# Performance work log

Measured on AMD Instinct MI355X. Metric: run time of the kernel, lower is better.

## Reference

```python
import jax, jax.numpy as jnp
import numpy as np
from jax import lax

B, C, T, V = 16, 3, 256, 25
MID = 48
DILS = (1, 2, 3, 4)
NB = len(DILS)
OUT = MID * NB
FH = [10, 100, 10, 1]
CH = [100]
EPS = 1e-5


def setup_inputs() -> dict:
    key = jax.random.key(0)
    ks = iter(jax.random.split(key, 64))
    nrm = lambda shape, s=0.05: jax.random.normal(next(ks), shape, jnp.float32) * s
    inp = {}
    inp['x'] = jax.random.normal(next(ks), (B, C, T, V), jnp.float32)
    # stacked per-timestep branch conv weights: (branch, v, mid, in=V, k=3)
    inp['Wb'] = nrm((NB, V, MID, V, 3))
    inp['bb'] = nrm((NB, V, MID))
    dims = [C] + FH
    for i in range(4):
        inp[f'fw{i}'] = nrm((dims[i + 1], dims[i]))
        inp[f'fb{i}'] = nrm((dims[i + 1],))
        inp[f'fg{i}'] = jnp.ones((dims[i + 1],), jnp.float32)
        inp[f'fbe{i}'] = jnp.zeros((dims[i + 1],), jnp.float32)
    cdims = [V] + CH + [OUT]
    for i in range(2):
        inp[f'cw{i}'] = nrm((cdims[i + 1], cdims[i]))
        inp[f'cb{i}'] = nrm((cdims[i + 1],))
        inp[f'cg{i}'] = jnp.ones((cdims[i + 1],), jnp.float32)
        inp[f'cbe{i}'] = jnp.zeros((cdims[i + 1],), jnp.float32)
    inp['Ww'] = nrm((V, OUT))  # branches_follow 1x1 conv weights (per v)
    inp['bw'] = nrm((V,))
    return inp


def _bn2d(y, g, b):
    m = y.mean((0, 2, 3), keepdims=True)
    v = ((y - m) ** 2).mean((0, 2, 3), keepdims=True)
    return g[None, :, None, None] * (y - m) / jnp.sqrt(v + EPS) + b[None, :, None, None]


def _bn1d(y, g, b):
    m = y.mean((0, 2), keepdims=True)
    v = ((y - m) ** 2).mean((0, 2), keepdims=True)
    return g[None, :, None] * (y - m) / jnp.sqrt(v + EPS) + b[None, :, None]


def reference(x, Wb, bb, fw0, fb0, fg0, fbe0, fw1, fb1, fg1, fbe1,
              fw2, fb2, fg2, fbe2, fw3, fb3, fg3, fbe3,
              cw0, cb0, cg0, cbe0, cw1, cb1, cg1, cbe1, Ww, bw):
    N = B * C
    x_temp = x.reshape(N, T, V).transpose(0, 2, 1)  # (N, V, T)
    # --- branches: 25 convs per branch fused as one big conv (out = V*MID) ---
    outs = []
    for i, d in enumerate(DILS):
        pad = 2 * d  # k + (k-1)(d-1) - 1 with k=3
        kern = Wb[i].reshape(V * MID, V, 3)
        y = lax.conv_general_dilated(x_temp, kern, window_strides=(1,),
                                     padding=[(pad, 0)], rhs_dilation=(d,),
                                     dimension_numbers=('NCH', 'OIH', 'NCH'))
        y = y + bb[i].reshape(V * MID)[None, :, None]  # (N, V*MID, T)
        # torch.cat over the 25 convs along time -> (N, MID, V*T)
        y = y.reshape(N, V, MID, T).transpose(0, 2, 1, 3).reshape(N, MID, V * T)
        outs.append(y)
    predic = jnp.stack(outs)  # (NB, N, MID, V*T)
    predic = predic.transpose(1, 0, 2, 3).reshape(N, NB * MID, V * T)
    predic = predic.reshape(N, -1, T, V).reshape(B, C, OUT, T, V)
    # --- feature branches (1x1 Conv2d + BN + ReLU chain) ---
    h = x
    for w, bi, g, be in ((fw0, fb0, fg0, fbe0), (fw1, fb1, fg1, fbe1),
                         (fw2, fb2, fg2, fbe2), (fw3, fb3, fg3, fbe3)):
        h = jnp.einsum('bctv,oc->botv', h, w) + bi[None, :, None, None]
        h = jax.nn.relu(_bn2d(h, g, be))
    h = h.reshape(-1, T, V).transpose(0, 2, 1).mean(-1, keepdims=True)  # (B, V, 1)
    # --- causal branches (1x1 Conv1d + BN + ReLU) ---
    for w, bi, g, be in ((cw0, cb0, cg0, cbe0), (cw1, cb1, cg1, cbe1)):
        h = jnp.einsum('bcl,oc->bol', h, w) + bi[None, :, None]
        h = jax.nn.relu(_bn1d(h, g, be))
    xg = h[:, :, :, None]  # (B, OUT, 1, 1)
    # --- gate, relu, per-timestep follow convs ---
    predic = predic * xg[:, None]  # (B, C, OUT, T, V)
    predic = jax.nn.relu(predic.reshape(N, OUT, T, V))
    predic_final = jnp.einsum('notv,vo->nvt', predic, Ww) + bw[None, :, None]  # (N, V, T)
    predic_loss = (predic_final[:, :, :-1] - x_temp[:, :, 1:]) ** 2  # MSE, no reduction
    # --- GC pool + regularization ---
    gc_pool = Wb.transpose(0, 2, 1, 3, 4).reshape(OUT, V, V, 3)
    gcw = gc_pool[None] * xg[:, :, :, :, None]  # (B, OUT, V, V, 3)
    lam = jnp.float32(0.01)
    reg = lam * (jnp.sum(jnp.sqrt(jnp.sum(gcw ** 2, axis=(1, 4)))) +
                 jnp.sum(jnp.sqrt(jnp.sum(gcw ** 2, axis=1))))
    gc = gcw.max(axis=1).max(axis=-1)  # (B, V, V)
    return (predic_loss, gc, reg)
```

## Files before the change

kernel.cpp:

```cpp
#include <hip/hip_runtime.h>

#define EPSV 1e-5f

constexpr int kB = 16, kC = 3, kT = 256, kV = 25;
constexpr int kMID = 48, kNB = 4, kOUT = 192, kN = 48;
constexpr int kS  = kB * kT * kV;
constexpr int kTV = kT * kV;

typedef __attribute__((ext_vector_type(8))) short bf16x8;
typedef __attribute__((ext_vector_type(4))) float f32x4;

__device__ __forceinline__ short f2bf(float f) {
  unsigned u = __float_as_uint(f);
  u += 0x7fffu + ((u >> 16) & 1u);
  return (short)(u >> 16);
}
__device__ __forceinline__ float bf2f(short s) {
  return __uint_as_float(((unsigned)(unsigned short)s) << 16);
}
__device__ __forceinline__ float wred(float v) {
  #pragma unroll
  for (int d = 32; d > 0; d >>= 1) v += __shfl_xor(v, d);
  return v;
}

__global__ __launch_bounds__(128) void xmom_kernel(const float* __restrict__ x,
                                                   float* __restrict__ xmom)
{
  __shared__ float red[9];
  const int tid = threadIdx.x;
  if (tid < 9) red[tid] = 0.f;
  __syncthreads();
  const int s = blockIdx.x * 128 + tid;
  const int b = s / kTV, r = s - b * kTV;
  const float x0 = x[(b * 3 + 0) * kTV + r];
  const float x1 = x[(b * 3 + 1) * kTV + r];
  const float x2 = x[(b * 3 + 2) * kTV + r];
  const float p[9] = {x0, x1, x2, x0*x0, x0*x1, x0*x2, x1*x1, x1*x2, x2*x2};
  #pragma unroll
  for (int k = 0; k < 9; k++) {
    float t = wred(p[k]);
    if ((tid & 63) == 0) atomicAdd(&red[k], t);
  }
  __syncthreads();
  if (tid < 9) atomicAdd(&xmom[tid], red[tid]);
}

__device__ __forceinline__ void st0_from_xmom(int o, const float* fw0, const float* fb0,
                                              const float* fg0, const float* fbe0,
                                              const float* xmom, float* sc0, float* sh0)
{
  float w0 = fw0[o * 3], w1 = fw0[o * 3 + 1], w2 = fw0[o * 3 + 2], b = fb0[o];
  float Sw = w0 * xmom[0] + w1 * xmom[1] + w2 * xmom[2];
  float Q  = w0*w0*xmom[3] + w1*w1*xmom[6] + w2*w2*xmom[8]
           + 2.f*(w0*w1*xmom[4] + w0*w2*xmom[5] + w1*w2*xmom[7]);
  float mean = (Sw + (float)kS * b) * (1.f / kS);
  float e2   = (Q + 2.f * b * Sw) * (1.f / kS) + b * b;
  float var  = e2 - mean * mean;
  float sc   = fg0[o] * rsqrtf(var + EPSV);
  sc0[o] = sc; sh0[o] = fbe0[o] - mean * sc;
}

__global__ __launch_bounds__(128) void h0mom_kernel(
    const float* __restrict__ x,
    const float* __restrict__ fw0, const float* __restrict__ fb0,
    const float* __restrict__ fg0, const float* __restrict__ fbe0,
    const float* __restrict__ xmom, float* __restrict__ h0mom)
{
  __shared__ __align__(16) float w0p[40];
  __shared__ float sc0[10], sh0[10];
  __shared__ float red[65];
  const int tid = threadIdx.x;
  for (int j = tid; j < 40; j += 128) {
    int o = j >> 2, c = j & 3;
    w0p[j] = (c < 3) ? fw0[o * 3 + c] : fb0[o];
  }
  if (tid < 10) st0_from_xmom(tid, fw0, fb0, fg0, fbe0, xmom, sc0, sh0);
  if (tid < 65) red[tid] = 0.f;
  __syncthreads();
  const int s = blockIdx.x * 128 + tid;
  const int b = s / kTV, r = s - b * kTV;
  const float x0 = x[(b * 3 + 0) * kTV + r];
  const float x1 = x[(b * 3 + 1) * kTV + r];
  const float x2 = x[(b * 3 + 2) * kTV + r];
  float h0[10];
  #pragma unroll
  for (int o = 0; o < 10; o++) {
    const float4 w = *(const float4*)&w0p[o * 4];
    float y = fmaf(x0, w.x, fmaf(x1, w.y, fmaf(x2, w.z, w.w)));
    h0[o] = fmaxf(fmaf(y, sc0[o], sh0[o]), 0.f);
  }
  int idx = 0;
  #pragma unroll
  for (int c = 0; c < 10; c++) {
    float t = wred(h0[c]);
    if ((tid & 63) == 0) atomicAdd(&red[idx], t);
    idx++;
  }
  #pragma unroll
  for (int c = 0; c < 10; c++)
    #pragma unroll
    for (int cp = c; cp < 10; cp++) {
      float t = wred(h0[c] * h0[cp]);
      if ((tid & 63) == 0) atomicAdd(&red[idx], t);
      idx++;
    }
  __syncthreads();
  if (tid < 65) atomicAdd(&h0mom[tid], red[tid]);
}

__global__ __launch_bounds__(128) void y2_kernel(
    const float* __restrict__ x,
    const float* __restrict__ fw0, const float* __restrict__ fb0,
    const float* __restrict__ fg0, const float* __restrict__ fbe0,
    const float* __restrict__ fw1, const float* __restrict__ fb1,
    const float* __restrict__ fg1, const float* __restrict__ fbe1,
    const float* __restrict__ fw2, const float* __restrict__ fb2,
    const float* __restrict__ xmom, const float* __restrict__ h0mom,
    short* __restrict__ y2out, float* __restrict__ st2out)
{
  __shared__ __align__(16) float w0p[40];
  __shared__ __align__(16) float w1p[1200];
  __shared__ __align__(16) float w2t[1200];
  __shared__ float b2s[10];
  __shared__ float sc0[10], sh0[10], sc1[100], sh1[100];
  __shared__ float red[20];
  const int tid = threadIdx.x;

  for (int j = tid; j < 40; j += 128) {
    int o = j >> 2, c = j & 3;
    w0p[j] = (c < 3) ? fw0[o * 3 + c] : fb0[o];
  }
  for (int j = tid; j < 1200; j += 128) {
    int o = j / 12, c = j - o * 12;
    w1p[j] = (c < 10) ? fw1[o * 10 + c] : (c == 10 ? fb1[o] : 0.f);
  }
  for (int j = tid; j < 1000; j += 128) {
    int jj = j / 100, c = j - jj * 100;
    w2t[c * 12 + jj] = fw2[j];
  }
  for (int c = tid; c < 100; c += 128) { w2t[c * 12 + 10] = 0.f; w2t[c * 12 + 11] = 0.f; }
  if (tid < 10) {
    b2s[tid] = fb2[tid];
    st0_from_xmom(tid, fw0, fb0, fg0, fbe0, xmom, sc0, sh0);
  }
  if (tid < 20) red[tid] = 0.f;
  __syncthreads();
  if (tid < 100) {
    float wr[10]; float S = 0.f, Q = 0.f;
    #pragma unroll
    for (int c = 0; c < 10; c++) { wr[c] = w1p[tid * 12 + c]; S = fmaf(wr[c], h0mom[c], S); }
    int idx = 10;
    #pragma unroll
    for (int c = 0; c < 10; c++) {
      Q = fmaf(wr[c] * wr[c], h0mom[idx], Q); idx++;
      #pragma unroll
      for (int cp = c + 1; cp < 10; cp++) { Q = fmaf(2.f * wr[c] * wr[cp], h0mom[idx], Q); idx++; }
    }
    float b = w1p[tid * 12 + 10];
    float mean = (S + (float)kS * b) * (1.f / kS);
    float e2   = (Q + 2.f * b * S) * (1.f / kS) + b * b;
    float var  = e2 - mean * mean;
    float sc   = fg1[tid] * rsqrtf(var + EPSV);
    sc1[tid] = sc; sh1[tid] = fbe1[tid] - mean * sc;
  }
  __syncthreads();

  const int s0 = blockIdx.x * 512 + tid;
  float h0a[4][10];
  #pragma unroll
  for (int k = 0; k < 4; k++) {
    const int s = s0 + k * 128;
    const int b = s / kTV, r = s - b * kTV;
    const float x0 = x[(b * 3 + 0) * kTV + r];
    const float x1 = x[(b * 3 + 1) * kTV + r];
    const float x2 = x[(b * 3 + 2) * kTV + r];
    #pragma unroll
    for (int o = 0; o < 10; o++) {
      const float4 w = *(const float4*)&w0p[o * 4];
      float y = fmaf(x0, w.x, fmaf(x1, w.y, fmaf(x2, w.z, w.w)));
      h0a[k][o] = fmaxf(fmaf(y, sc0[o], sh0[o]), 0.f);
    }
  }
  float acc[4][10];
  #pragma unroll
  for (int k = 0; k < 4; k++)
    #pragma unroll
    for (int o = 0; o < 10; o++) acc[k][o] = b2s[o];

  #pragma unroll 2
  for (int o = 0; o < 100; o++) {
    const float4 wa = *(const float4*)&w1p[o * 12];
    const float4 wb = *(const float4*)&w1p[o * 12 + 4];
    const float4 wc = *(const float4*)&w1p[o * 12 + 8];
    const float4 va = *(const float4*)&w2t[o * 12];
    const float4 vb = *(const float4*)&w2t[o * 12 + 4];
    const float4 vc = *(const float4*)&w2t[o * 12 + 8];
    const float sc = sc1[o], sh = sh1[o];
    #pragma unroll
    for (int k = 0; k < 4; k++) {
      float a = wc.z;
      a = fmaf(h0a[k][0], wa.x, a); a = fmaf(h0a[k][1], wa.y, a);
      a = fmaf(h0a[k][2], wa.z, a); a = fmaf(h0a[k][3], wa.w, a);
      a = fmaf(h0a[k][4], wb.x, a); a = fmaf(h0a[k][5], wb.y, a);
      a = fmaf(h0a[k][6], wb.z, a); a = fmaf(h0a[k][7], wb.w, a);
      a = fmaf(h0a[k][8], wc.x, a); a = fmaf(h0a[k][9], wc.y, a);
      const float h1 = fmaxf(fmaf(a, sc, sh), 0.f);
      acc[k][0] = fmaf(h1, va.x, acc[k][0]); acc[k][1] = fmaf(h1, va.y, acc[k][1]);
      acc[k][2] = fmaf(h1, va.z, acc[k][2]); acc[k][3] = fmaf(h1, va.w, acc[k][3]);
      acc[k][4] = fmaf(h1, vb.x, acc[k][4]); acc[k][5] = fmaf(h1, vb.y, acc[k][5]);
      acc[k][6] = fmaf(h1, vb.z, acc[k][6]); acc[k][7] = fmaf(h1, vb.w, acc[k][7]);
      acc[k][8] = fmaf(h1, vc.x, acc[k][8]); acc[k][9] = fmaf(h1, vc.y, acc[k][9]);
    }
  }

  #pragma unroll
  for (int k = 0; k < 4; k++) {
    const int s = s0 + k * 128;
    #pragma unroll
    for (int o = 0; o < 10; o++) y2out[o * kS + s] = f2bf(acc[k][o]);
  }
  #pragma unroll
  for (int o = 0; o < 10; o++) {
    float s1 = acc[0][o] + acc[1][o] + acc[2][o] + acc[3][o];
    float s2 = acc[0][o]*acc[0][o] + acc[1][o]*acc[1][o] + acc[2][o]*acc[2][o] + acc[3][o]*acc[3][o];
    s1 = wred(s1); s2 = wred(s2);
    if ((tid & 63) == 0) { atomicAdd(&red[2 * o], s1); atomicAdd(&red[2 * o + 1], s2); }
  }
  __syncthreads();
  if (tid < 20) atomicAdd(&st2out[tid], red[tid]);
}

__global__ __launch_bounds__(128) void y3_kernel(
    const short* __restrict__ y2,
    const float* __restrict__ fw3, const float* __restrict__ fb3,
    const float* __restrict__ fg2, const float* __restrict__ fbe2,
    const float* __restrict__ st2,
    float* __restrict__ y3out, float* __restrict__ st3out)
{
  __shared__ float sc2[10], sh2[10], w3s[10];
  __shared__ float b3s;
  __shared__ float red[2];
  const int tid = threadIdx.x;
  if (tid < 10) {
    float m  = st2[2 * tid] * (1.f / kS);
    float vr = st2[2 * tid + 1] * (1.f / kS) - m * m;
    float sc = fg2[tid] * rsqrtf(vr + EPSV);
    sc2[tid] = sc; sh2[tid] = fbe2[tid] - m * sc;
    w3s[tid] = fw3[tid];
  }
  if (tid == 0) b3s = fb3[0];
  if (tid < 2) red[tid] = 0.f;
  __syncthreads();
  const int s = blockIdx.x * 128 + tid;
  float y3 = b3s;
  #pragma unroll
  for (int o = 0; o < 10; o++) {
    float v = bf2f(y2[o * kS + s]);
    float h2 = fmaxf(fmaf(v, sc2[o], sh2[o]), 0.f);
    y3 = fmaf(h2, w3s[o], y3);
  }
  y3out[s] = y3;
  float s1 = wred(y3), s2 = wred(y3 * y3);
  if ((tid & 63) == 0) { atomicAdd(&red[0], s1); atomicAdd(&red[1], s2); }
  __syncthreads();
  if (tid < 2) atomicAdd(&st3out[tid], red[tid]);
}

__global__ __launch_bounds__(128) void pool5_kernel(
    const float* __restrict__ y3,
    const float* __restrict__ fg3, const float* __restrict__ fbe3,
    const float* __restrict__ st3, float* __restrict__ hp)
{
  __shared__ float scsh[2];
  __shared__ float poolp[25];
  const int tid = threadIdx.x;
  if (tid == 0) {
    float m  = st3[0] * (1.f / kS);
    float vr = st3[1] * (1.f / kS) - m * m;
    float sc = fg3[0] * rsqrtf(vr + EPSV);
    scsh[0] = sc; scsh[1] = fbe3[0] - m * sc;
  }
  if (tid < 25) poolp[tid] = 0.f;
  __syncthreads();
  const int s = blockIdx.x * 128 + tid;
  const int b = s / kTV, r = s - b * kTV;
  const int v = r % 25;
  float h3 = fmaxf(fmaf(y3[s], scsh[0], scsh[1]), 0.f);
  atomicAdd(&poolp[v], h3);
  __syncthreads();
  if (tid < 25) atomicAdd(&hp[b * 25 + tid], poolp[tid]);
}

__global__ __launch_bounds__(256) void head_kernel(
    const float* __restrict__ hp,
    const float* __restrict__ cw0, const float* __restrict__ cb0,
    const float* __restrict__ cg0, const float* __restrict__ cbe0,
    const float* __restrict__ cw1, const float* __restrict__ cb1,
    const float* __restrict__ cg1, const float* __restrict__ cbe1,
    float* __restrict__ xg, float* __restrict__ xgT)
{
  __shared__ float hpl[400];
  __shared__ float y1[100 * 16];
  __shared__ float y2l[192 * 16];
  const int tid = threadIdx.x;
  for (int j = tid; j < 400; j += 256) hpl[j] = hp[j] * (1.f / kT);
  __syncthreads();
  for (int j = tid; j < 1600; j += 256) {
    int o = j >> 4, b = j & 15;
    float acc = cb0[o];
    for (int v = 0; v < 25; v++) acc = fmaf(hpl[b * 25 + v], cw0[o * 25 + v], acc);
    y1[o * 16 + b] = acc;
  }
  __syncthreads();
  if (tid < 100) {
    float s1 = 0.f, s2 = 0.f;
    for (int b = 0; b < 16; b++) { float val = y1[tid * 16 + b]; s1 += val; s2 += val * val; }
    float m = s1 * (1.f / 16), vr = s2 * (1.f / 16) - m * m;
    float scale = cg0[tid] * rsqrtf(vr + EPSV);
    float shift = cbe0[tid] - m * scale;
    for (int b = 0; b < 16; b++)
      y1[tid * 16 + b] = fmaxf(fmaf(y1[tid * 16 + b], scale, shift), 0.f);
  }
  __syncthreads();
  for (int j = tid; j < 3072; j += 256) {
    int o = j >> 4, b = j & 15;
    float acc = cb1[o];
    for (int c = 0; c < 100; c++) acc = fmaf(y1[c * 16 + b], cw1[o * 100 + c], acc);
    y2l[o * 16 + b] = acc;
  }
  __syncthreads();
  if (tid < 192) {
    float s1 = 0.f, s2 = 0.f;
    for (int b = 0; b < 16; b++) { float val = y2l[tid * 16 + b]; s1 += val; s2 += val * val; }
    float m = s1 * (1.f / 16), vr = s2 * (1.f / 16) - m * m;
    float scale = cg1[tid] * rsqrtf(vr + EPSV);
    float shift = cbe1[tid] - m * scale;
    for (int b = 0; b < 16; b++) {
      float r = fmaxf(fmaf(y2l[tid * 16 + b], scale, shift), 0.f);
      xg[b * 192 + tid]  = r;
      xgT[tid * 16 + b]  = r;
    }
  }
}

__global__ __launch_bounds__(256) void conv_fuse_mfma(
    const float* __restrict__ x, const float* __restrict__ Wb,
    const float* __restrict__ bb, const float* __restrict__ Ww,
    const float* __restrict__ bw, const float* __restrict__ xg,
    float* __restrict__ out_loss)
{
  __shared__ short xs[264 * 40];
  __shared__ short As[48 * 104];
  __shared__ float gw[25 * 200];
  __shared__ float bbl[192], bwl[32];

  const int tid = threadIdx.x;
  const int v = blockIdx.x % 25, n = blockIdx.x / 25;
  const int bidx = n / 3;

  {
    uint2* p = (uint2*)xs;
    for (int j = tid; j < 2640; j += 256) p[j] = make_uint2(0u, 0u);
    uint2* p2 = (uint2*)As;
    for (int j = tid; j < 1248; j += 256) p2[j] = make_uint2(0u, 0u);
  }
  __syncthreads();
  for (int j = tid; j < 6400; j += 256) {
    int t = j / 25, ci = j - t * 25;
    xs[(8 + t) * 40 + ci] = f2bf(x[n * 6400 + j]);
  }
  for (int j = tid; j < 4800; j += 256) {
    int vv = j / 192, o = j - vv * 192;
    gw[vv * 200 + o] = xg[bidx * 192 + o] * Ww[j];
  }
  for (int j = tid; j < 192; j += 256) {
    int i = j / 48, m = j - i * 48;
    bbl[j] = bb[(i * 25 + v) * 48 + m];
  }
  if (tid < 25) bwl[tid] = bw[tid];

  const int lane = tid & 63, w = tid >> 6;
  const int c = lane & 15, q = lane >> 4;

  float accout[4] = {0.f, 0.f, 0.f, 0.f};
  int tarr[4], vparr[4];
  #pragma unroll
  for (int z = 0; z < 4; z++) {
    int t = (w * 4 + z) * 16 + c;
    tarr[z] = t;
    vparr[z] = (v * 256 + t) % 25;
  }

  for (int i = 0; i < 4; i++) {
    __syncthreads();
    const float* wsrc = Wb + (i * 25 + v) * 3600;
    for (int j = tid; j < 3600; j += 256) {
      int m = j / 75, r = j - m * 75;
      int ci = r / 3, k = r - ci * 3;
      As[m * 104 + k * 32 + ci] = f2bf(wsrc[j]);
    }
    __syncthreads();

    const int d = i + 1;
    bf16x8 af[3][3];
    #pragma unroll
    for (int mt = 0; mt < 3; mt++)
      #pragma unroll
      for (int s = 0; s < 3; s++)
        af[mt][s] = *(const bf16x8*)&As[(mt * 16 + c) * 104 + s * 32 + q * 8];

    #pragma unroll
    for (int z = 0; z < 4; z++) {
      const int t = tarr[z];
      bf16x8 bf[3];
      #pragma unroll
      for (int s = 0; s < 3; s++) {
        int row = 8 + t + (s - 2) * d;
        bf[s] = *(const bf16x8*)&xs[row * 40 + q * 8];
      }
      f32x4 acc[3] = {{0.f,0.f,0.f,0.f},{0.f,0.f,0.f,0.f},{0.f,0.f,0.f,0.f}};
      #pragma unroll
      for (int s = 0; s < 3; s++)
        #pragma unroll
        for (int mt = 0; mt < 3; mt++)
          acc[mt] = __builtin_amdgcn_mfma_f32_16x16x32_bf16(af[mt][s], bf[s], acc[mt], 0, 0, 0);
      const int vp = vparr[z];
      float aout = 0.f;
      #pragma unroll
      for (int mt = 0; mt < 3; mt++) {
        #pragma unroll
        for (int r = 0; r < 4; r++) {
          int o = i * 48 + mt * 16 + q * 4 + r;
          float val = acc[mt][r] + bbl[o];
          aout = fmaf(fmaxf(val, 0.f), gw[vp * 200 + o], aout);
        }
      }
      accout[z] += aout;
    }
  }

  #pragma unroll
  for (int z = 0; z < 4; z++) {
    float a = accout[z];
    a += __shfl_xor(a, 16);
    a += __shfl_xor(a, 32);
    if (q == 0) {
      int flat = v * 256 + tarr[z];
      int tp = flat / 25, vp = flat - tp * 25;
      if (tp < 255) {
        float pf = a + bwl[vp];
        float xn = x[n * 6400 + (tp + 1) * 25 + vp];
        float dd = pf - xn;
        out_loss[(n * 25 + vp) * 255 + tp] = dd * dd;
      }
    }
  }
}

__global__ __launch_bounds__(64) void gc_reg_kernel(
    const float* __restrict__ Wb, const float* __restrict__ xgT,
    float* __restrict__ gc_out, float* __restrict__ reg_out)
{
  __shared__ float sW[576];
  __shared__ float sG[192 * 17];
  const int tid = threadIdx.x;
  const int v1 = blockIdx.x / 25, v2 = blockIdx.x % 25;
  for (int j = tid; j < 3072; j += 64) {
    int o = j >> 4, bq = j & 15;
    sG[o * 17 + bq] = xgT[j];
  }
  for (int p = tid; p < 192; p += 64) {
    int i = p / 48, m = p - i * 48;
    const float* src = Wb + ((i * 25 + v1) * 48 + m) * 75 + v2 * 3;
    sW[p * 3 + 0] = src[0]; sW[p * 3 + 1] = src[1]; sW[p * 3 + 2] = src[2];
  }
  __syncthreads();
  const int b = tid & 15, c = tid >> 4;
  float s0 = 0.f, s1 = 0.f, s2 = 0.f, mx = -3.0e38f;
  #pragma unroll 4
  for (int o = c * 48; o < c * 48 + 48; o++) {
    float g = sG[o * 17 + b];
    float a0 = sW[o * 3] * g, a1 = sW[o * 3 + 1] * g, a2 = sW[o * 3 + 2] * g;
    s0 = fmaf(a0, a0, s0);
    s1 = fmaf(a1, a1, s1);
    s2 = fmaf(a2, a2, s2);
    mx = fmaxf(mx, fmaxf(fmaxf(a0, a1), a2));
  }
  s0 += __shfl_xor(s0, 16); s0 += __shfl_xor(s0, 32);
  s1 += __shfl_xor(s1, 16); s1 += __shfl_xor(s1, 32);
  s2 += __shfl_xor(s2, 16); s2 += __shfl_xor(s2, 32);
  mx = fmaxf(mx, __shfl_xor(mx, 16)); mx = fmaxf(mx, __shfl_xor(mx, 32));
  float contrib = 0.f;
  if (c == 0) {
    gc_out[(b * 25 + v1) * 25 + v2] = mx;
    contrib = sqrtf(s0 + s1 + s2) + sqrtf(s0) + sqrtf(s1) + sqrtf(s2);
  }
  #pragma unroll
  for (int d = 1; d < 16; d <<= 1) contrib += __shfl_xor(contrib, d);
  if (tid == 0) atomicAdd(reg_out, 0.01f * contrib);
}

extern "C" void kernel_launch(void* const* d_in, const int* in_sizes, int n_in,
                              void* d_out, int out_size, void* d_ws, size_t ws_size,
                              hipStream_t stream)
{
  const float* x    = (const float*)d_in[0];
  const float* Wb   = (const float*)d_in[1];
  const float* bb   = (const float*)d_in[2];
  const float* fw0  = (const float*)d_in[3];
  const float* fb0  = (const float*)d_in[4];
  const float* fg0  = (const float*)d_in[5];
  const float* fbe0 = (const float*)d_in[6];
  const float* fw1  = (const float*)d_in[7];
  const float* fb1  = (const float*)d_in[8];
  const float* fg1  = (const float*)d_in[9];
  const float* fbe1 = (const float*)d_in[10];
  const float* fw2  = (const float*)d_in[11];
  const float* fb2  = (const float*)d_in[12];
  const float* fg2  = (const float*)d_in[13];
  const float* fbe2 = (const float*)d_in[14];
  const float* fw3  = (const float*)d_in[15];
  const float* fb3  = (const float*)d_in[16];
  const float* fg3  = (const float*)d_in[17];
  const float* fbe3 = (const float*)d_in[18];
  const float* cw0  = (const float*)d_in[19];
  const float* cb0  = (const float*)d_in[20];
  const float* cg0  = (const float*)d_in[21];
  const float* cbe0 = (const float*)d_in[22];
  const float* cw1  = (const float*)d_in[23];
  const float* cb1  = (const float*)d_in[24];
  const float* cg1  = (const float*)d_in[25];
  const float* cbe1 = (const float*)d_in[26];
  const float* Ww   = (const float*)d_in[27];
  const float* bw   = (const float*)d_in[28];

  float* ws  = (float*)d_ws;
  float* out = (float*)d_out;

  float* XMOM  = ws;
  float* H0MOM = ws + 16;
  float* ST2   = ws + 296;
  float* ST3   = ws + 316;
  float* HP    = ws + 320;
  float* XG    = ws + 768;
  float* XGT   = ws + 3840;
  short* Y2    = (short*)(ws + 8192);
  float* Y3    = ws + 520192;

  hipMemsetAsync(ws, 0, 720 * sizeof(float), stream);
  hipMemsetAsync(out + 316000, 0, sizeof(float), stream);

  xmom_kernel<<<800, 128, 0, stream>>>(x, XMOM);
  h0mom_kernel<<<800, 128, 0, stream>>>(x, fw0, fb0, fg0, fbe0, XMOM, H0MOM);
  y2_kernel<<<200, 128, 0, stream>>>(x, fw0, fb0, fg0, fbe0, fw1, fb1, fg1, fbe1,
      fw2, fb2, XMOM, H0MOM, Y2, ST2);
  y3_kernel<<<800, 128, 0, stream>>>(Y2, fw3, fb3, fg2, fbe2, ST2, Y3, ST3);
  pool5_kernel<<<800, 128, 0, stream>>>(Y3, fg3, fbe3, ST3, HP);
  head_kernel<<<1, 256, 0, stream>>>(HP, cw0, cb0, cg0, cbe0, cw1, cb1, cg1, cbe1, XG, XGT);
  conv_fuse_mfma<<<1200, 256, 0, stream>>>(x, Wb, bb, Ww, bw, XG, out);
  gc_reg_kernel<<<625, 64, 0, stream>>>(Wb, XGT, out + 306000, out + 316000);
}
```

Baseline: 165.2 us.

## Fuse pre-conv stages into one cooperative kernel with grid syncs

Merges the moment, feature-MLP, BN-stat, pooling, head and GC/regularization kernels into a single cooperative kernel of 256 blocks that uses grid.sync between stages. Y2/Y3 no longer round-trip through global memory because activations stay in registers. The same kernel also pre-converts x and Wb into padded bf16 layouts and precomputes the gated follow weights, so the MFMA conv kernel only does vector copies. This removes several launches and intermediate traffic, at the cost of grid-wide barriers, lower occupancy and serial head work on one block.

```diff
diff --git a/kernel.cpp b/kernel.cpp
--- a/kernel.cpp
+++ b/kernel.cpp
@@ -1,4 +1,7 @@
 #include <hip/hip_runtime.h>
+#include <hip/hip_cooperative_groups.h>
+
+namespace cg = cooperative_groups;
 
 #define EPSV 1e-5f
 
@@ -15,36 +18,20 @@
   u += 0x7fffu + ((u >> 16) & 1u);
   return (short)(u >> 16);
 }
-__device__ __forceinline__ float bf2f(short s) {
-  return __uint_as_float(((unsigned)(unsigned short)s) << 16);
-}
 __device__ __forceinline__ float wred(float v) {
   #pragma unroll
   for (int d = 32; d > 0; d >>= 1) v += __shfl_xor(v, d);
   return v;
 }
 
-__global__ __launch_bounds__(128) void xmom_kernel(const float* __restrict__ x,
-                                                   float* __restrict__ xmom)
-{
-  __shared__ float red[9];
-  const int tid = threadIdx.x;
-  if (tid < 9) red[tid] = 0.f;
-  __syncthreads();
-  const int s = blockIdx.x * 128 + tid;
-  const int b = s / kTV, r = s - b * kTV;
-  const float x0 = x[(b * 3 + 0) * kTV + r];
-  const float x1 = x[(b * 3 + 1) * kTV + r];
-  const float x2 = x[(b * 3 + 2) * kTV + r];
-  const float p[9] = {x0, x1, x2, x0*x0, x0*x1, x0*x2, x1*x1, x1*x2, x2*x2};
-  #pragma unroll
-  for (int k = 0; k < 9; k++) {
-    float t = wred(p[k]);
-    if ((tid & 63) == 0) atomicAdd(&red[k], t);
-  }
-  __syncthreads();
-  if (tid < 9) atomicAdd(&xmom[tid], red[tid]);
-}
+struct Params {
+  const float *x, *Wb, *bb;
+  const float *fw0,*fb0,*fg0,*fbe0, *fw1,*fb1,*fg1,*fbe1;
+  const float *fw2,*fb2,*fg2,*fbe2, *fw3,*fb3,*fg3,*fbe3;
+  const float *cw0,*cb0,*cg0,*cbe0, *cw1,*cb1,*cg1,*cbe1;
+  const float *Ww,*bw;
+  float* ws; float* out;
+};
 
 __device__ __forceinline__ void st0_from_xmom(int o, const float* fw0, const float* fb0,
                                               const float* fg0, const float* fbe0,
@@ -61,144 +48,175 @@
   sc0[o] = sc; sh0[o] = fbe0[o] - mean * sc;
 }
 
-__global__ __launch_bounds__(128) void h0mom_kernel(
-    const float* __restrict__ x,
-    const float* __restrict__ fw0, const float* __restrict__ fb0,
-    const float* __restrict__ fg0, const float* __restrict__ fbe0,
-    const float* __restrict__ xmom, float* __restrict__ h0mom)
+__global__ __launch_bounds__(256) void fused_pre(Params p)
 {
+  cg::grid_group grid = cg::this_grid();
+  const int tid = threadIdx.x, bid = blockIdx.x;
+  const int gtid = bid * 256 + tid;
+
+  float* XMOM  = p.ws;
+  float* H0MOM = p.ws + 16;
+  float* ST2   = p.ws + 112;
+  float* ST3   = p.ws + 132;
+  float* HP    = p.ws + 144;
+  float* XG    = p.ws + 544;
+  float* XGT   = p.ws + 3616;
+  float* GW    = p.ws + 8192;
+  short* WBBF  = (short*)(p.ws + 88192);
+  short* XSG   = (short*)(p.ws + 337792);
+
+  __shared__ float l_red[65];
   __shared__ __align__(16) float w0p[40];
   __shared__ float sc0[10], sh0[10];
-  __shared__ float red[65];
-  const int tid = threadIdx.x;
-  for (int j = tid; j < 40; j += 128) {
+  __shared__ __align__(16) float w1p[1200];
+  __shared__ __align__(16) float w2t[1200];
+  __shared__ float sc1[100], sh1[100];
+  __shared__ float b2s[10];
+  __shared__ float sc2[10], sh2[10], w3s[12];
+  __shared__ float st3l[2];
+  __shared__ float sG[192 * 17];
+  __shared__ float hpl[400];
+  __shared__ float y1h[1600];
+  __shared__ float y2h[3072];
+
+  for (int j = gtid; j < 48 * 10560; j += 65536) {
+    int n = j / 10560, rem = j - n * 10560;
+    int row = rem / 40, ci = rem - row * 40;
+    short val = 0;
+    if (row >= 8 && ci < 25) val = f2bf(p.x[n * 6400 + (row - 8) * 25 + ci]);
+    XSG[j] = val;
+  }
+  for (int j = gtid; j < 499200; j += 65536) {
+    int g = j / 4992, rem = j - g * 4992;
+    int m = rem / 104, kk = rem - m * 104;
+    int k = kk >> 5, ci = kk & 31;
+    short val = 0;
+    if (ci < 25 && kk < 96) val = f2bf(p.Wb[g * 3600 + m * 75 + ci * 3 + k]);
+    WBBF[j] = val;
+  }
+
+  const int s0_ = gtid, s1_ = gtid + 65536;
+  const bool ns2 = (s1_ < kS);
+  float xv[2][3] = {{0.f,0.f,0.f},{0.f,0.f,0.f}};
+  {
+    int b0 = s0_ / kTV, r0 = s0_ - b0 * kTV;
+    xv[0][0] = p.x[(b0*3+0)*kTV + r0];
+    xv[0][1] = p.x[(b0*3+1)*kTV + r0];
+    xv[0][2] = p.x[(b0*3+2)*kTV + r0];
+    if (ns2) {
+      int b1 = s1_ / kTV, r1 = s1_ - b1 * kTV;
+      xv[1][0] = p.x[(b1*3+0)*kTV + r1];
+      xv[1][1] = p.x[(b1*3+1)*kTV + r1];
+      xv[1][2] = p.x[(b1*3+2)*kTV + r1];
+    }
+  }
+  for (int j = tid; j < 9; j += 256) l_red[j] = 0.f;
+  __syncthreads();
+  {
+    float pm[9];
+    pm[0] = xv[0][0]+xv[1][0]; pm[1] = xv[0][1]+xv[1][1]; pm[2] = xv[0][2]+xv[1][2];
+    pm[3] = xv[0][0]*xv[0][0]+xv[1][0]*xv[1][0];
+    pm[4] = xv[0][0]*xv[0][1]+xv[1][0]*xv[1][1];
+    pm[5] = xv[0][0]*xv[0][2]+xv[1][0]*xv[1][2];
+    pm[6] = xv[0][1]*xv[0][1]+xv[1][1]*xv[1][1];
+    pm[7] = xv[0][1]*xv[0][2]+xv[1][1]*xv[1][2];
+    pm[8] = xv[0][2]*xv[0][2]+xv[1][2]*xv[1][2];
+    #pragma unroll
+    for (int k = 0; k < 9; k++) {
+      float t = wred(pm[k]);
+      if ((tid & 63) == 0) atomicAdd(&l_red[k], t);
+    }
+  }
+  __syncthreads();
+  if (tid < 9) atomicAdd(&XMOM[tid], l_red[tid]);
+  grid.sync();
+
+  if (tid < 10) st0_from_xmom(tid, p.fw0, p.fb0, p.fg0, p.fbe0, XMOM, sc0, sh0);
+  for (int j = tid; j < 40; j += 256) {
     int o = j >> 2, c = j & 3;
-    w0p[j] = (c < 3) ? fw0[o * 3 + c] : fb0[o];
-  }
-  if (tid < 10) st0_from_xmom(tid, fw0, fb0, fg0, fbe0, xmom, sc0, sh0);
-  if (tid < 65) red[tid] = 0.f;
-  __syncthreads();
-  const int s = blockIdx.x * 128 + tid;
-  const int b = s / kTV, r = s - b * kTV;
-  const float x0 = x[(b * 3 + 0) * kTV + r];
-  const float x1 = x[(b * 3 + 1) * kTV + r];
-  const float x2 = x[(b * 3 + 2) * kTV + r];
-  float h0[10];
+    w0p[j] = (c < 3) ? p.fw0[o * 3 + c] : p.fb0[o];
+  }
+  for (int j = tid; j < 65; j += 256) l_red[j] = 0.f;
+  __syncthreads();
+  float h0a[2][10];
   #pragma unroll
   for (int o = 0; o < 10; o++) {
     const float4 w = *(const float4*)&w0p[o * 4];
-    float y = fmaf(x0, w.x, fmaf(x1, w.y, fmaf(x2, w.z, w.w)));
-    h0[o] = fmaxf(fmaf(y, sc0[o], sh0[o]), 0.f);
-  }
-  int idx = 0;
-  #pragma unroll
-  for (int c = 0; c < 10; c++) {
-    float t = wred(h0[c]);
-    if ((tid & 63) == 0) atomicAdd(&red[idx], t);
-    idx++;
-  }
-  #pragma unroll
-  for (int c = 0; c < 10; c++)
-    #pragma unroll
-    for (int cp = c; cp < 10; cp++) {
-      float t = wred(h0[c] * h0[cp]);
-      if ((tid & 63) == 0) atomicAdd(&red[idx], t);
+    float y0 = fmaf(xv[0][0], w.x, fmaf(xv[0][1], w.y, fmaf(xv[0][2], w.z, w.w)));
+    h0a[0][o] = fmaxf(fmaf(y0, sc0[o], sh0[o]), 0.f);
+    if (ns2) {
+      float y1v = fmaf(xv[1][0], w.x, fmaf(xv[1][1], w.y, fmaf(xv[1][2], w.z, w.w)));
+      h0a[1][o] = fmaxf(fmaf(y1v, sc0[o], sh0[o]), 0.f);
+    } else h0a[1][o] = 0.f;
+  }
+  {
+    int idx = 0;
+    #pragma unroll
+    for (int c = 0; c < 10; c++) {
+      float t = wred(h0a[0][c] + h0a[1][c]);
+      if ((tid & 63) == 0) atomicAdd(&l_red[idx], t);
       idx++;
     }
-  __syncthreads();
-  if (tid < 65) atomicAdd(&h0mom[tid], red[tid]);
-}
-
-__global__ __launch_bounds__(128) void y2_kernel(
-    const float* __restrict__ x,
-    const float* __restrict__ fw0, const float* __restrict__ fb0,
-    const float* __restrict__ fg0, const float* __restrict__ fbe0,
-    const float* __restrict__ fw1, const float* __restrict__ fb1,
-    const float* __restrict__ fg1, const float* __restrict__ fbe1,
-    const float* __restrict__ fw2, const float* __restrict__ fb2,
-    const float* __restrict__ xmom, const float* __restrict__ h0mom,
-    short* __restrict__ y2out, float* __restrict__ st2out)
-{
-  __shared__ __align__(16) float w0p[40];
-  __shared__ __align__(16) float w1p[1200];
-  __shared__ __align__(16) float w2t[1200];
-  __shared__ float b2s[10];
-  __shared__ float sc0[10], sh0[10], sc1[100], sh1[100];
-  __shared__ float red[20];
-  const int tid = threadIdx.x;
-
-  for (int j = tid; j < 40; j += 128) {
-    int o = j >> 2, c = j & 3;
-    w0p[j] = (c < 3) ? fw0[o * 3 + c] : fb0[o];
-  }
-  for (int j = tid; j < 1200; j += 128) {
+    #pragma unroll
+    for (int c = 0; c < 10; c++)
+      #pragma unroll
+      for (int cp = c; cp < 10; cp++) {
+        float t = wred(h0a[0][c]*h0a[0][cp] + h0a[1][c]*h0a[1][cp]);
+        if ((tid & 63) == 0) atomicAdd(&l_red[idx], t);
+        idx++;
+      }
+  }
+  __syncthreads();
+  if (tid < 65) atomicAdd(&H0MOM[tid], l_red[tid]);
+  grid.sync();
+
+  for (int j = tid; j < 1200; j += 256) {
     int o = j / 12, c = j - o * 12;
-    w1p[j] = (c < 10) ? fw1[o * 10 + c] : (c == 10 ? fb1[o] : 0.f);
-  }
-  for (int j = tid; j < 1000; j += 128) {
+    w1p[j] = (c < 10) ? p.fw1[o * 10 + c] : (c == 10 ? p.fb1[o] : 0.f);
+  }
+  for (int j = tid; j < 1000; j += 256) {
     int jj = j / 100, c = j - jj * 100;
-    w2t[c * 12 + jj] = fw2[j];
-  }
-  for (int c = tid; c < 100; c += 128) { w2t[c * 12 + 10] = 0.f; w2t[c * 12 + 11] = 0.f; }
-  if (tid < 10) {
-    b2s[tid] = fb2[tid];
-    st0_from_xmom(tid, fw0, fb0, fg0, fbe0, xmom, sc0, sh0);
-  }
-  if (tid < 20) red[tid] = 0.f;
+    w2t[c * 12 + jj] = p.fw2[j];
+  }
+  for (int c = tid; c < 100; c += 256) { w2t[c*12+10] = 0.f; w2t[c*12+11] = 0.f; }
+  if (tid < 10) b2s[tid] = p.fb2[tid];
+  for (int j = tid; j < 20; j += 256) l_red[j] = 0.f;
   __syncthreads();
   if (tid < 100) {
     float wr[10]; float S = 0.f, Q = 0.f;
     #pragma unroll
-    for (int c = 0; c < 10; c++) { wr[c] = w1p[tid * 12 + c]; S = fmaf(wr[c], h0mom[c], S); }
+    for (int c = 0; c < 10; c++) { wr[c] = w1p[tid*12+c]; S = fmaf(wr[c], H0MOM[c], S); }
     int idx = 10;
     #pragma unroll
     for (int c = 0; c < 10; c++) {
-      Q = fmaf(wr[c] * wr[c], h0mom[idx], Q); idx++;
-      #pragma unroll
-      for (int cp = c + 1; cp < 10; cp++) { Q = fmaf(2.f * wr[c] * wr[cp], h0mom[idx], Q); idx++; }
-    }
-    float b = w1p[tid * 12 + 10];
+      Q = fmaf(wr[c]*wr[c], H0MOM[idx], Q); idx++;
+      #pragma unroll
+      for (int cp = c + 1; cp < 10; cp++) { Q = fmaf(2.f*wr[c]*wr[cp], H0MOM[idx], Q); idx++; }
+    }
+    float b = w1p[tid*12+10];
     float mean = (S + (float)kS * b) * (1.f / kS);
     float e2   = (Q + 2.f * b * S) * (1.f / kS) + b * b;
     float var  = e2 - mean * mean;
-    float sc   = fg1[tid] * rsqrtf(var + EPSV);
-    sc1[tid] = sc; sh1[tid] = fbe1[tid] - mean * sc;
-  }
-  __syncthreads();
-
-  const int s0 = blockIdx.x * 512 + tid;
-  float h0a[4][10];
-  #pragma unroll
-  for (int k = 0; k < 4; k++) {
-    const int s = s0 + k * 128;
-    const int b = s / kTV, r = s - b * kTV;
-    const float x0 = x[(b * 3 + 0) * kTV + r];
-    const float x1 = x[(b * 3 + 1) * kTV + r];
-    const float x2 = x[(b * 3 + 2) * kTV + r];
-    #pragma unroll
-    for (int o = 0; o < 10; o++) {
-      const float4 w = *(const float4*)&w0p[o * 4];
-      float y = fmaf(x0, w.x, fmaf(x1, w.y, fmaf(x2, w.z, w.w)));
-      h0a[k][o] = fmaxf(fmaf(y, sc0[o], sh0[o]), 0.f);
-    }
-  }
-  float acc[4][10];
-  #pragma unroll
-  for (int k = 0; k < 4; k++)
+    float sc   = p.fg1[tid] * rsqrtf(var + EPSV);
+    sc1[tid] = sc; sh1[tid] = p.fbe1[tid] - mean * sc;
+  }
+  __syncthreads();
+  float acc[2][10];
+  #pragma unroll
+  for (int k = 0; k < 2; k++)
     #pragma unroll
     for (int o = 0; o < 10; o++) acc[k][o] = b2s[o];
-
   #pragma unroll 2
   for (int o = 0; o < 100; o++) {
-    const float4 wa = *(const float4*)&w1p[o * 12];
-    const float4 wb = *(const float4*)&w1p[o * 12 + 4];
-    const float4 wc = *(const float4*)&w1p[o * 12 + 8];
-    const float4 va = *(const float4*)&w2t[o * 12];
-    const float4 vb = *(const float4*)&w2t[o * 12 + 4];
-    const float4 vc = *(const float4*)&w2t[o * 12 + 8];
+    const float4 wa = *(const float4*)&w1p[o*12];
+    const float4 wb = *(const float4*)&w1p[o*12+4];
+    const float4 wc = *(const float4*)&w1p[o*12+8];
+    const float4 va = *(const float4*)&w2t[o*12];
+    const float4 vb = *(const float4*)&w2t[o*12+4];
+    const float4 vc = *(const float4*)&w2t[o*12+8];
     const float sc = sc1[o], sh = sh1[o];
     #pragma unroll
-    for (int k = 0; k < 4; k++) {
+    for (int k = 0; k < 2; k++) {
       float a = wc.z;
       a = fmaf(h0a[k][0], wa.x, a); a = fmaf(h0a[k][1], wa.y, a);
       a = fmaf(h0a[k][2], wa.z, a); a = fmaf(h0a[k][3], wa.w, a);
@@ -213,146 +231,156 @@
       acc[k][8] = fmaf(h1, vc.x, acc[k][8]); acc[k][9] = fmaf(h1, vc.y, acc[k][9]);
     }
   }
-
-  #pragma unroll
-  for (int k = 0; k < 4; k++) {
-    const int s = s0 + k * 128;
-    #pragma unroll
-    for (int o = 0; o < 10; o++) y2out[o * kS + s] = f2bf(acc[k][o]);
-  }
   #pragma unroll
   for (int o = 0; o < 10; o++) {
-    float s1 = acc[0][o] + acc[1][o] + acc[2][o] + acc[3][o];
-    float s2 = acc[0][o]*acc[0][o] + acc[1][o]*acc[1][o] + acc[2][o]*acc[2][o] + acc[3][o]*acc[3][o];
-    s1 = wred(s1); s2 = wred(s2);
-    if ((tid & 63) == 0) { atomicAdd(&red[2 * o], s1); atomicAdd(&red[2 * o + 1], s2); }
-  }
-  __syncthreads();
-  if (tid < 20) atomicAdd(&st2out[tid], red[tid]);
+    float a1 = acc[0][o] + (ns2 ? acc[1][o] : 0.f);
+    float a2 = acc[0][o]*acc[0][o] + (ns2 ? acc[1][o]*acc[1][o] : 0.f);
+    a1 = wred(a1); a2 = wred(a2);
+    if ((tid & 63) == 0) { atomicAdd(&l_red[2*o], a1); atomicAdd(&l_red[2*o+1], a2); }
+  }
+  __syncthreads();
+  if (tid < 20) atomicAdd(&ST2[tid], l_red[tid]);
+  grid.sync();
+
+  if (tid < 10) {
+    float m  = ST2[2*tid] * (1.f / kS);
+    float vr = ST2[2*tid+1] * (1.f / kS) - m * m;
+    float sc = p.fg2[tid] * rsqrtf(vr + EPSV);
+    sc2[tid] = sc; sh2[tid] = p.fbe2[tid] - m * sc;
+  }
+  if (tid < 12) w3s[tid] = (tid < 10) ? p.fw3[tid] : (tid == 10 ? p.fb3[0] : 0.f);
+  if (tid < 2) l_red[tid] = 0.f;
+  __syncthreads();
+  float y3v[2];
+  #pragma unroll
+  for (int k = 0; k < 2; k++) {
+    float y3 = w3s[10];
+    #pragma unroll
+    for (int o = 0; o < 10; o++) {
+      float h2 = fmaxf(fmaf(acc[k][o], sc2[o], sh2[o]), 0.f);
+      y3 = fmaf(h2, w3s[o], y3);
+    }
+    y3v[k] = y3;
+  }
+  {
+    float a1 = y3v[0] + (ns2 ? y3v[1] : 0.f);
+    float a2 = y3v[0]*y3v[0] + (ns2 ? y3v[1]*y3v[1] : 0.f);
+    a1 = wred(a1); a2 = wred(a2);
+    if ((tid & 63) == 0) { atomicAdd(&l_red[0], a1); atomicAdd(&l_red[1], a2); }
+  }
+  __syncthreads();
+  if (tid < 2) atomicAdd(&ST3[tid], l_red[tid]);
+  grid.sync();
+
+  if (tid == 0) {
+    float m  = ST3[0] * (1.f / kS);
+    float vr = ST3[1] * (1.f / kS) - m * m;
+    float sc = p.fg3[0] * rsqrtf(vr + EPSV);
+    st3l[0] = sc; st3l[1] = p.fbe3[0] - m * sc;
+  }
+  __syncthreads();
+  {
+    int b0 = s0_ / kTV, r0 = s0_ - b0 * kTV;
+    float h3 = fmaxf(fmaf(y3v[0], st3l[0], st3l[1]), 0.f);
+    atomicAdd(&HP[b0 * 25 + r0 % 25], h3);
+    if (ns2) {
+      int b1 = s1_ / kTV, r1 = s1_ - b1 * kTV;
+      float h3b = fmaxf(fmaf(y3v[1], st3l[0], st3l[1]), 0.f);
+      atomicAdd(&HP[b1 * 25 + r1 % 25], h3b);
+    }
+  }
+  grid.sync();
+
+  if (bid == 0) {
+    for (int j = tid; j < 400; j += 256) hpl[j] = HP[j] * (1.f / kT);
+    __syncthreads();
+    for (int j = tid; j < 1600; j += 256) {
+      int o = j >> 4, b = j & 15;
+      float a = p.cb0[o];
+      for (int v = 0; v < 25; v++) a = fmaf(hpl[b*25+v], p.cw0[o*25+v], a);
+      y1h[o*16+b] = a;
+    }
+    __syncthreads();
+    if (tid < 100) {
+      float a1 = 0.f, a2 = 0.f;
+      for (int b = 0; b < 16; b++) { float val = y1h[tid*16+b]; a1 += val; a2 += val*val; }
+      float m = a1 * (1.f/16), vr = a2 * (1.f/16) - m*m;
+      float scale = p.cg0[tid] * rsqrtf(vr + EPSV);
+      float shift = p.cbe0[tid] - m * scale;
+      for (int b = 0; b < 16; b++)
+        y1h[tid*16+b] = fmaxf(fmaf(y1h[tid*16+b], scale, shift), 0.f);
+    }
+    __syncthreads();
+    for (int j = tid; j < 3072; j += 256) {
+      int o = j >> 4, b = j & 15;
+      float a = p.cb1[o];
+      for (int c = 0; c < 100; c++) a = fmaf(y1h[c*16+b], p.cw1[o*100+c], a);
+      y2h[o*16+b] = a;
+    }
+    __syncthreads();
+    if (tid < 192) {
+      float a1 = 0.f, a2 = 0.f;
+      for (int b = 0; b < 16; b++) { float val = y2h[tid*16+b]; a1 += val; a2 += val*val; }
+      float m = a1 * (1.f/16), vr = a2 * (1.f/16) - m*m;
+      float scale = p.cg1[tid] * rsqrtf(vr + EPSV);
+      float shift = p.cbe1[tid] - m * scale;
+      for (int b = 0; b < 16; b++) {
+        float r = fmaxf(fmaf(y2h[tid*16+b], scale, shift), 0.f);
+        XG[b*192+tid]  = r;
+        XGT[tid*16+b]  = r;
+      }
+    }
+  }
+  grid.sync();
+
+  for (int j = gtid; j < 80000; j += 65536) {
+    int bidx = j / 5000, rem = j - bidx * 5000;
+    int vp = rem / 200, o = rem - vp * 200;
+    GW[j] = (o < 192) ? XG[bidx*192+o] * p.Ww[vp*192+o] : 0.f;
+  }
+  for (int j = tid; j < 3072; j += 256) sG[(j>>4)*17 + (j&15)] = XGT[j];
+  __syncthreads();
+  {
+    const int lane = tid & 63, wave = tid >> 6;
+    const int u = bid * 4 + wave;
+    if (u < 625) {
+      const int v1 = u / 25, v2 = u - v1 * 25;
+      const int b = lane & 15, c = lane >> 4;
+      float q0 = 0.f, q1 = 0.f, q2 = 0.f, mx = -3.0e38f;
+      const float* wbase = p.Wb + ((c*25+v1)*48)*75 + v2*3;
+      #pragma unroll 4
+      for (int m = 0; m < 48; m++) {
+        const float* w3 = wbase + m * 75;
+        float g = sG[(c*48+m)*17 + b];
+        float a0 = w3[0]*g, a1 = w3[1]*g, a2 = w3[2]*g;
+        q0 = fmaf(a0, a0, q0); q1 = fmaf(a1, a1, q1); q2 = fmaf(a2, a2, q2);
+        mx = fmaxf(mx, fmaxf(fmaxf(a0, a1), a2));
+      }
+      q0 += __shfl_xor(q0, 16); q0 += __shfl_xor(q0, 32);
+      q1 += __shfl_xor(q1, 16); q1 += __shfl_xor(q1, 32);
+      q2 += __shfl_xor(q2, 16); q2 += __shfl_xor(q2, 32);
+      mx = fmaxf(mx, __shfl_xor(mx, 16)); mx = fmaxf(mx, __shfl_xor(mx, 32));
+      float contrib = 0.f;
+      if (c == 0) {
+        p.out[306000 + (b*25+v1)*25 + v2] = mx;
+        contrib = sqrtf(q0+q1+q2) + sqrtf(q0) + sqrtf(q1) + sqrtf(q2);
+      }
+      #pragma unroll
+      for (int d = 1; d < 16; d <<= 1) contrib += __shfl_xor(contrib, d);
+      if (lane == 0) atomicAdd(&p.out[316000], 0.01f * contrib);
+    }
+  }
 }
 
-__global__ __launch_bounds__(128) void y3_kernel(
-    const short* __restrict__ y2,
-    const float* __restrict__ fw3, const float* __restrict__ fb3,
-    const float* __restrict__ fg2, const float* __restrict__ fbe2,
-    const float* __restrict__ st2,
-    float* __restrict__ y3out, float* __restrict__ st3out)
-{
-  __shared__ float sc2[10], sh2[10], w3s[10];
-  __shared__ float b3s;
-  __shared__ float red[2];
-  const int tid = threadIdx.x;
-  if (tid < 10) {
-    float m  = st2[2 * tid] * (1.f / kS);
-    float vr = st2[2 * tid + 1] * (1.f / kS) - m * m;
-    float sc = fg2[tid] * rsqrtf(vr + EPSV);
-    sc2[tid] = sc; sh2[tid] = fbe2[tid] - m * sc;
-    w3s[tid] = fw3[tid];
-  }
-  if (tid == 0) b3s = fb3[0];
-  if (tid < 2) red[tid] = 0.f;
-  __syncthreads();
-  const int s = blockIdx.x * 128 + tid;
-  float y3 = b3s;
-  #pragma unroll
-  for (int o = 0; o < 10; o++) {
-    float v = bf2f(y2[o * kS + s]);
-    float h2 = fmaxf(fmaf(v, sc2[o], sh2[o]), 0.f);
-    y3 = fmaf(h2, w3s[o], y3);
-  }
-  y3out[s] = y3;
-  float s1 = wred(y3), s2 = wred(y3 * y3);
-  if ((tid & 63) == 0) { atomicAdd(&red[0], s1); atomicAdd(&red[1], s2); }
-  __syncthreads();
-  if (tid < 2) atomicAdd(&st3out[tid], red[tid]);
-}
-
-__global__ __launch_bounds__(128) void pool5_kernel(
-    const float* __restrict__ y3,
-    const float* __restrict__ fg3, const float* __restrict__ fbe3,
-    const float* __restrict__ st3, float* __restrict__ hp)
-{
-  __shared__ float scsh[2];
-  __shared__ float poolp[25];
-  const int tid = threadIdx.x;
-  if (tid == 0) {
-    float m  = st3[0] * (1.f / kS);
-    float vr = st3[1] * (1.f / kS) - m * m;
-    float sc = fg3[0] * rsqrtf(vr + EPSV);
-    scsh[0] = sc; scsh[1] = fbe3[0] - m * sc;
-  }
-  if (tid < 25) poolp[tid] = 0.f;
-  __syncthreads();
-  const int s = blockIdx.x * 128 + tid;
-  const int b = s / kTV, r = s - b * kTV;
-  const int v = r % 25;
-  float h3 = fmaxf(fmaf(y3[s], scsh[0], scsh[1]), 0.f);
-  atomicAdd(&poolp[v], h3);
-  __syncthreads();
-  if (tid < 25) atomicAdd(&hp[b * 25 + tid], poolp[tid]);
-}
-
-__global__ __launch_bounds__(256) void head_kernel(
-    const float* __restrict__ hp,
-    const float* __restrict__ cw0, const float* __restrict__ cb0,
-    const float* __restrict__ cg0, const float* __restrict__ cbe0,
-    const float* __restrict__ cw1, const float* __restrict__ cb1,
-    const float* __restrict__ cg1, const float* __restrict__ cbe1,
-    float* __restrict__ xg, float* __restrict__ xgT)
-{
-  __shared__ float hpl[400];
-  __shared__ float y1[100 * 16];
-  __shared__ float y2l[192 * 16];
-  const int tid = threadIdx.x;
-  for (int j = tid; j < 400; j += 256) hpl[j] = hp[j] * (1.f / kT);
-  __syncthreads();
-  for (int j = tid; j < 1600; j += 256) {
-    int o = j >> 4, b = j & 15;
-    float acc = cb0[o];
-    for (int v = 0; v < 25; v++) acc = fmaf(hpl[b * 25 + v], cw0[o * 25 + v], acc);
-    y1[o * 16 + b] = acc;
-  }
-  __syncthreads();
-  if (tid < 100) {
-    float s1 = 0.f, s2 = 0.f;
-    for (int b = 0; b < 16; b++) { float val = y1[tid * 16 + b]; s1 += val; s2 += val * val; }
-    float m = s1 * (1.f / 16), vr = s2 * (1.f / 16) - m * m;
-    float scale = cg0[tid] * rsqrtf(vr + EPSV);
-    float shift = cbe0[tid] - m * scale;
-    for (int b = 0; b < 16; b++)
-      y1[tid * 16 + b] = fmaxf(fmaf(y1[tid * 16 + b], scale, shift), 0.f);
-  }
-  __syncthreads();
-  for (int j = tid; j < 3072; j += 256) {
-    int o = j >> 4, b = j & 15;
-    float acc = cb1[o];
-    for (int c = 0; c < 100; c++) acc = fmaf(y1[c * 16 + b], cw1[o * 100 + c], acc);
-    y2l[o * 16 + b] = acc;
-  }
-  __syncthreads();
-  if (tid < 192) {
-    float s1 = 0.f, s2 = 0.f;
-    for (int b = 0; b < 16; b++) { float val = y2l[tid * 16 + b]; s1 += val; s2 += val * val; }
-    float m = s1 * (1.f / 16), vr = s2 * (1.f / 16) - m * m;
-    float scale = cg1[tid] * rsqrtf(vr + EPSV);
-    float shift = cbe1[tid] - m * scale;
-    for (int b = 0; b < 16; b++) {
-      float r = fmaxf(fmaf(y2l[tid * 16 + b], scale, shift), 0.f);
-      xg[b * 192 + tid]  = r;
-      xgT[tid * 16 + b]  = r;
-    }
-  }
-}
-
 __global__ __launch_bounds__(256) void conv_fuse_mfma(
-    const float* __restrict__ x, const float* __restrict__ Wb,
-    const float* __restrict__ bb, const float* __restrict__ Ww,
-    const float* __restrict__ bw, const float* __restrict__ xg,
+    const short* __restrict__ XSG, const short* __restrict__ WBBF,
+    const float* __restrict__ GW, const float* __restrict__ x,
+    const float* __restrict__ bb, const float* __restrict__ bw,
     float* __restrict__ out_loss)
 {
-  __shared__ short xs[264 * 40];
-  __shared__ short As[48 * 104];
-  __shared__ float gw[25 * 200];
+  __shared__ __align__(16) short xs[264 * 40];
+  __shared__ __align__(16) short As[48 * 104];
+  __shared__ __align__(16) float gw[5000];
   __shared__ float bbl[192], bwl[32];
 
   const int tid = threadIdx.x;
@@ -360,19 +388,14 @@
   const int bidx = n / 3;
 
   {
-    uint2* p = (uint2*)xs;
-    for (int j = tid; j < 2640; j += 256) p[j] = make_uint2(0u, 0u);
-    uint2* p2 = (uint2*)As;
-    for (int j = tid; j < 1248; j += 256) p2[j] = make_uint2(0u, 0u);
-  }
-  __syncthreads();
-  for (int j = tid; j < 6400; j += 256) {
-    int t = j / 25, ci = j - t * 25;
-    xs[(8 + t) * 40 + ci] = f2bf(x[n * 6400 + j]);
-  }
-  for (int j = tid; j < 4800; j += 256) {
-    int vv = j / 192, o = j - vv * 192;
-    gw[vv * 200 + o] = xg[bidx * 192 + o] * Ww[j];
+    const uint4* src = (const uint4*)(XSG + n * 10560);
+    uint4* dst = (uint4*)xs;
+    for (int j = tid; j < 1320; j += 256) dst[j] = src[j];
+  }
+  {
+    const float4* src = (const float4*)(GW + bidx * 5000);
+    float4* dst = (float4*)gw;
+    for (int j = tid; j < 1250; j += 256) dst[j] = src[j];
   }
   for (int j = tid; j < 192; j += 256) {
     int i = j / 48, m = j - i * 48;
@@ -394,11 +417,10 @@
 
   for (int i = 0; i < 4; i++) {
     __syncthreads();
-    const float* wsrc = Wb + (i * 25 + v) * 3600;
-    for (int j = tid; j < 3600; j += 256) {
-      int m = j / 75, r = j - m * 75;
-      int ci = r / 3, k = r - ci * 3;
-      As[m * 104 + k * 32 + ci] = f2bf(wsrc[j]);
+    {
+      const uint4* src = (const uint4*)(WBBF + (i * 25 + v) * 4992);
+      uint4* dst = (uint4*)As;
+      for (int j = tid; j < 624; j += 256) dst[j] = src[j];
     }
     __syncthreads();
 
@@ -413,18 +435,18 @@
     #pragma unroll
     for (int z = 0; z < 4; z++) {
       const int t = tarr[z];
-      bf16x8 bf[3];
+      bf16x8 bfv[3];
       #pragma unroll
       for (int s = 0; s < 3; s++) {
         int row = 8 + t + (s - 2) * d;
-        bf[s] = *(const bf16x8*)&xs[row * 40 + q * 8];
+        bfv[s] = *(const bf16x8*)&xs[row * 40 + q * 8];
       }
       f32x4 acc[3] = {{0.f,0.f,0.f,0.f},{0.f,0.f,0.f,0.f},{0.f,0.f,0.f,0.f}};
       #pragma unroll
       for (int s = 0; s < 3; s++)
         #pragma unroll
         for (int mt = 0; mt < 3; mt++)
-          acc[mt] = __builtin_amdgcn_mfma_f32_16x16x32_bf16(af[mt][s], bf[s], acc[mt], 0, 0, 0);
+          acc[mt] = __builtin_amdgcn_mfma_f32_16x16x32_bf16(af[mt][s], bfv[s], acc[mt], 0, 0, 0);
       const int vp = vparr[z];
       float aout = 0.f;
       #pragma unroll
@@ -458,106 +480,53 @@
   }
 }
 
-__global__ __launch_bounds__(64) void gc_reg_kernel(
-    const float* __restrict__ Wb, const float* __restrict__ xgT,
-    float* __restrict__ gc_out, float* __restrict__ reg_out)
-{
-  __shared__ float sW[576];
-  __shared__ float sG[192 * 17];
-  const int tid = threadIdx.x;
-  const int v1 = blockIdx.x / 25, v2 = blockIdx.x % 25;
-  for (int j = tid; j < 3072; j += 64) {
-    int o = j >> 4, bq = j & 15;
-    sG[o * 17 + bq] = xgT[j];
-  }
-  for (int p = tid; p < 192; p += 64) {
-    int i = p / 48, m = p - i * 48;
-    const float* src = Wb + ((i * 25 + v1) * 48 + m) * 75 + v2 * 3;
-    sW[p * 3 + 0] = src[0]; sW[p * 3 + 1] = src[1]; sW[p * 3 + 2] = src[2];
-  }
-  __syncthreads();
-  const int b = tid & 15, c = tid >> 4;
-  float s0 = 0.f, s1 = 0.f, s2 = 0.f, mx = -3.0e38f;
-  #pragma unroll 4
-  for (int o = c * 48; o < c * 48 + 48; o++) {
-    float g = sG[o * 17 + b];
-    float a0 = sW[o * 3] * g, a1 = sW[o * 3 + 1] * g, a2 = sW[o * 3 + 2] * g;
-    s0 = fmaf(a0, a0, s0);
-    s1 = fmaf(a1, a1, s1);
-    s2 = fmaf(a2, a2, s2);
-    mx = fmaxf(mx, fmaxf(fmaxf(a0, a1), a2));
-  }
-  s0 += __shfl_xor(s0, 16); s0 += __shfl_xor(s0, 32);
-  s1 += __shfl_xor(s1, 16); s1 += __shfl_xor(s1, 32);
-  s2 += __shfl_xor(s2, 16); s2 += __shfl_xor(s2, 32);
-  mx = fmaxf(mx, __shfl_xor(mx, 16)); mx = fmaxf(mx, __shfl_xor(mx, 32));
-  float contrib = 0.f;
-  if (c == 0) {
-    gc_out[(b * 25 + v1) * 25 + v2] = mx;
-    contrib = sqrtf(s0 + s1 + s2) + sqrtf(s0) + sqrtf(s1) + sqrtf(s2);
-  }
-  #pragma unroll
-  for (int d = 1; d < 16; d <<= 1) contrib += __shfl_xor(contrib, d);
-  if (tid == 0) atomicAdd(reg_out, 0.01f * contrib);
-}
-
 extern "C" void kernel_launch(void* const* d_in, const int* in_sizes, int n_in,
                               void* d_out, int out_size, void* d_ws, size_t ws_size,
                               hipStream_t stream)
 {
-  const float* x    = (const float*)d_in[0];
-  const float* Wb   = (const float*)d_in[1];
-  const float* bb   = (const float*)d_in[2];
-  const float* fw0  = (const float*)d_in[3];
-  const float* fb0  = (const float*)d_in[4];
-  const float* fg0  = (const float*)d_in[5];
-  const float* fbe0 = (const float*)d_in[6];
-  const float* fw1  = (const float*)d_in[7];
-  const float* fb1  = (const float*)d_in[8];
-  const float* fg1  = (const float*)d_in[9];
-  const float* fbe1 = (const float*)d_in[10];
-  const float* fw2  = (const float*)d_in[11];
-  const float* fb2  = (const float*)d_in[12];
-  const float* fg2  = (const float*)d_in[13];
-  const float* fbe2 = (const float*)d_in[14];
-  const float* fw3  = (const float*)d_in[15];
-  const float* fb3  = (const float*)d_in[16];
-  const float* fg3  = (const float*)d_in[17];
-  const float* fbe3 = (const float*)d_in[18];
-  const float* cw0  = (const float*)d_in[19];
-  const float* cb0  = (const float*)d_in[20];
-  const float* cg0  = (const float*)d_in[21];
-  const float* cbe0 = (const float*)d_in[22];
-  const float* cw1  = (const float*)d_in[23];
-  const float* cb1  = (const float*)d_in[24];
-  const float* cg1  = (const float*)d_in[25];
-  const float* cbe1 = (const float*)d_in[26];
-  const float* Ww   = (const float*)d_in[27];
-  const float* bw   = (const float*)d_in[28];
+  Params prm;
+  prm.x    = (const float*)d_in[0];
+  prm.Wb   = (const float*)d_in[1];
+  prm.bb   = (const float*)d_in[2];
+  prm.fw0  = (const float*)d_in[3];
+  prm.fb0  = (const float*)d_in[4];
+  prm.fg0  = (const float*)d_in[5];
+  prm.fbe0 = (const float*)d_in[6];
+  prm.fw1  = (const float*)d_in[7];
+  prm.fb1  = (const float*)d_in[8];
+  prm.fg1  = (const float*)d_in[9];
+  prm.fbe1 = (const float*)d_in[10];
+  prm.fw2  = (const float*)d_in[11];
+  prm.fb2  = (const float*)d_in[12];
+  prm.fg2  = (const float*)d_in[13];
+  prm.fbe2 = (const float*)d_in[14];
+  prm.fw3  = (const float*)d_in[15];
+  prm.fb3  = (const float*)d_in[16];
+  prm.fg3  = (const float*)d_in[17];
+  prm.fbe3 = (const float*)d_in[18];
+  prm.cw0  = (const float*)d_in[19];
+  prm.cb0  = (const float*)d_in[20];
+  prm.cg0  = (const float*)d_in[21];
+  prm.cbe0 = (const float*)d_in[22];
+  prm.cw1  = (const float*)d_in[23];
+  prm.cb1  = (const float*)d_in[24];
+  prm.cg1  = (const float*)d_in[25];
+  prm.cbe1 = (const float*)d_in[26];
+  prm.Ww   = (const float*)d_in[27];
+  prm.bw   = (const float*)d_in[28];
+  prm.ws   = (float*)d_ws;
+  prm.out  = (float*)d_out;
 
   float* ws  = (float*)d_ws;
   float* out = (float*)d_out;
 
-  float* XMOM  = ws;
-  float* H0MOM = ws + 16;
-  float* ST2   = ws + 296;
-  float* ST3   = ws + 316;
-  float* HP    = ws + 320;
-  float* XG    = ws + 768;
-  float* XGT   = ws + 3840;
-  short* Y2    = (short*)(ws + 8192);
-  float* Y3    = ws + 520192;
-
-  hipMemsetAsync(ws, 0, 720 * sizeof(float), stream);
+  hipMemsetAsync(ws, 0, 8192 * sizeof(float), stream);
   hipMemsetAsync(out + 316000, 0, sizeof(float), stream);
 
-  xmom_kernel<<<800, 128, 0, stream>>>(x, XMOM);
-  h0mom_kernel<<<800, 128, 0, stream>>>(x, fw0, fb0, fg0, fbe0, XMOM, H0MOM);
-  y2_kernel<<<200, 128, 0, stream>>>(x, fw0, fb0, fg0, fbe0, fw1, fb1, fg1, fbe1,
-      fw2, fb2, XMOM, H0MOM, Y2, ST2);
-  y3_kernel<<<800, 128, 0, stream>>>(Y2, fw3, fb3, fg2, fbe2, ST2, Y3, ST3);
-  pool5_kernel<<<800, 128, 0, stream>>>(Y3, fg3, fbe3, ST3, HP);
-  head_kernel<<<1, 256, 0, stream>>>(HP, cw0, cb0, cg0, cbe0, cw1, cb1, cg1, cbe1, XG, XGT);
-  conv_fuse_mfma<<<1200, 256, 0, stream>>>(x, Wb, bb, Ww, bw, XG, out);
-  gc_reg_kernel<<<625, 64, 0, stream>>>(Wb, XGT, out + 306000, out + 316000);
+  void* args[] = { &prm };
+  hipLaunchCooperativeKernel((const void*)fused_pre, dim3(256), dim3(256), args, 0, stream);
+
+  conv_fuse_mfma<<<1200, 256, 0, stream>>>(
+      (const short*)(ws + 337792), (const short*)(ws + 88192),
+      ws + 8192, prm.x, prm.bb, prm.bw, out);
 }
```

New measurement: 286.7 us. +73.5%, slower.
